# Optimization experiments

Measured on AMD Instinct MI355X. Metric: run time of the kernel, lower is better.

Reference implementation:

```python
import jax, jax.numpy as jnp
import numpy as np


def setup_inputs() -> dict:
    key = jax.random.key(0)
    ks = jax.random.split(key, 16)
    B, S, D, H = 32, 2048, 512, 512
    s = 1.0 / np.sqrt(H)
    inp = {
        "x": jax.random.normal(ks[0], (B, H), jnp.float32),
        "context": jax.random.normal(ks[1], (B, S, D), jnp.float32),
        "mask": jnp.zeros((B, S), jnp.bool_),  # False = valid position
        "Wi": jax.random.normal(ks[2], (H, H), jnp.float32) * s,
        "bi": jax.random.normal(ks[3], (H,), jnp.float32) * s,
        "Wc0": jax.random.normal(ks[4], (H, D), jnp.float32) * s,
        "bc0": jax.random.normal(ks[5], (H,), jnp.float32) * s,
        "Wc1": jax.random.normal(ks[6], (H, D), jnp.float32) * s,
        "bc1": jax.random.normal(ks[7], (H,), jnp.float32) * s,
        "Wc2": jax.random.normal(ks[8], (H, D), jnp.float32) * s,
        "bc2": jax.random.normal(ks[9], (H,), jnp.float32) * s,
        "Wc3": jax.random.normal(ks[10], (H, D), jnp.float32) * s,
        "bc3": jax.random.normal(ks[11], (H,), jnp.float32) * s,
        "V": jax.random.uniform(ks[12], (H,), jnp.float32, -s, s),
    }
    return inp


def reference(x, context, mask, Wi, bi, Wc0, bc0, Wc1, bc1, Wc2, bc2, Wc3, bc3, V):
    # mask: True = masked out in the original API; module flips it first.
    valid = ~mask  # [B, S], True = keep

    inp = (x @ Wi.T + bi)[:, :, None]  # [B, H, 1]

    def proj(W, b):
        # Conv1d(D, H, kernel=1) on context.permute(0,2,1) == token-wise GEMM
        return jnp.einsum("bsd,hd->bhs", context, W) + b[None, :, None]  # [B, H, S]

    ctx = jnp.concatenate(
        [proj(Wc0, bc0), proj(Wc1, bc1), proj(Wc2, bc2), proj(Wc3, bc3)], axis=2
    )  # [B, H, 4S]

    t = jnp.tanh(inp + ctx)                      # [B, H, 4S]
    att = jnp.einsum("h,bhs->bs", V, t)          # bmm(V[B,1,H], t).squeeze(1)
    att = 10.0 * jnp.tanh(att)                   # [B, 4S]

    valid4 = jnp.tile(valid, (1, 4))             # mask.repeat(1, 4)
    att = jnp.where(valid4, att, -jnp.inf)
    # torch.no_grad() around the masked fill detaches the rest of the graph
    att = jax.lax.stop_gradient(att)

    ans = jax.nn.softmax(att, axis=1)            # [B, 4S]
    p = jnp.max(ans, axis=1)
    indices = jnp.argmax(ans, axis=1)
    return indices[:, None], p[:, None], mask
```

## Files before the change

### kernel.cpp

```cpp
#include <hip/hip_runtime.h>
#include <math.h>

typedef __bf16 bf16x8 __attribute__((ext_vector_type(8)));
typedef float f32x4 __attribute__((ext_vector_type(4)));
typedef short short8v __attribute__((ext_vector_type(8)));

#define MARGIN 0.01f
#define NCAND 32

#define WAITL do { asm volatile("s_waitcnt lgkmcnt(0)" ::: "memory"); __builtin_amdgcn_sched_barrier(0); } while (0)
#define WAITV do { asm volatile("s_waitcnt vmcnt(0)" ::: "memory"); __builtin_amdgcn_sched_barrier(0); } while (0)
#define RBAR  do { __builtin_amdgcn_sched_barrier(0); __builtin_amdgcn_s_barrier(); } while (0)
#define BARR  __builtin_amdgcn_s_barrier()

#define MFMA_PHASE(NH, B0, B1) do { \
    WAITL; \
    __builtin_amdgcn_s_setprio(1); \
    _Pragma("unroll") \
    for (int mi = 0; mi < 8; ++mi) { \
      acc[mi][2*(NH)]   = __builtin_amdgcn_mfma_f32_16x16x32_bf16(a[mi], (B0), acc[mi][2*(NH)],   0, 0, 0); \
      acc[mi][2*(NH)+1] = __builtin_amdgcn_mfma_f32_16x16x32_bf16(a[mi], (B1), acc[mi][2*(NH)+1], 0, 0, 0); \
    } \
    __builtin_amdgcn_s_setprio(0); \
  } while (0)

__device__ __forceinline__ unsigned short f2bf(float f) {
  unsigned u = __float_as_uint(f);
  u += 0x7fffu + ((u >> 16) & 1u);
  return (unsigned short)(u >> 16);
}
__device__ __forceinline__ float tanh_fast(float x) {
  float e = __builtin_amdgcn_exp2f(x * 2.885390081777927f);
  return 1.f - 2.f * __builtin_amdgcn_rcpf(e + 1.f);
}
__device__ __forceinline__ void gl_lds16(const void* g, void* l) {
  __builtin_amdgcn_global_load_lds(
      (const __attribute__((address_space(1))) unsigned int*)g,
      (__attribute__((address_space(3))) unsigned int*)l, 16, 0, 0);
}

__global__ __launch_bounds__(256) void prep_inp_k(const float* __restrict__ x,
    const float* __restrict__ Wi, const float* __restrict__ bi, float* __restrict__ inp) {
  int gid = blockIdx.x * 256 + threadIdx.x;
  int b = gid >> 9, h = gid & 511;
  const float* xr = x + b * 512;
  const float* wr = Wi + h * 512;
  float acc = bi[h];
  #pragma unroll 4
  for (int k = 0; k < 512; k += 4) {
    float4 xv = *(const float4*)(xr + k);
    float4 wv = *(const float4*)(wr + k);
    acc += xv.x * wv.x + xv.y * wv.y + xv.z * wv.z + xv.w * wv.w;
  }
  inp[gid] = acc;
}

__global__ __launch_bounds__(256) void prep_w_pack_k(const float* __restrict__ w0,
    const float* __restrict__ w1, const float* __restrict__ w2, const float* __restrict__ w3,
    short* __restrict__ Whi) {
  int gid = blockIdx.x * 256 + threadIdx.x;
  if (gid >= 131072) return;
  int s = gid & 7, r = (gid >> 3) & 255, KT = (gid >> 11) & 7, TN = gid >> 14;
  int n = TN * 256 + r;
  int g = n >> 9, h = n & 511;
  const float* w = (g == 0) ? w0 : (g == 1) ? w1 : (g == 2) ? w2 : w3;
  int k = KT * 64 + ((s ^ (r & 7)) * 8);
  float f[8];
  *(float4*)&f[0] = *(const float4*)(w + (size_t)h * 512 + k);
  *(float4*)&f[4] = *(const float4*)(w + (size_t)h * 512 + k + 4);
  short8v hv;
  #pragma unroll
  for (int i = 0; i < 8; ++i) hv[i] = (short)f2bf(f[i]);
  *(short8v*)(Whi + (size_t)gid * 8) = hv;
}

__global__ __launch_bounds__(256) void prep_ctx_pack_k(const float* __restrict__ ctx,
    short* __restrict__ Chi) {
  int gid = blockIdx.x * 256 + threadIdx.x;
  int s = gid & 7, r = (gid >> 3) & 255, KT = (gid >> 11) & 7, TM = gid >> 14;
  size_t m = (size_t)TM * 256 + r;
  int k = KT * 64 + ((s ^ (r & 7)) * 8);
  float f[8];
  *(float4*)&f[0] = *(const float4*)(ctx + m * 512 + k);
  *(float4*)&f[4] = *(const float4*)(ctx + m * 512 + k + 4);
  short8v hv;
  #pragma unroll
  for (int i = 0; i < 8; ++i) hv[i] = (short)f2bf(f[i]);
  *(short8v*)(Chi + (size_t)gid * 8) = hv;
}

template<bool PRESPLIT>
__global__ __launch_bounds__(512, 2) void gemm_att_k(
    const float* __restrict__ ctx, const short* __restrict__ Chi,
    const short* __restrict__ Whi,
    const float* __restrict__ inp,
    const float* __restrict__ bc0, const float* __restrict__ bc1,
    const float* __restrict__ bc2, const float* __restrict__ bc3,
    const float* __restrict__ V, float* __restrict__ att) {
  __shared__ __align__(16) short smem[2][2][16384];
  __shared__ float sV[256], sPre[256];

  const int t = threadIdx.x;
  int d = blockIdx.x + (blockIdx.y << 3);
  int work = (d & 7) * 256 + (d >> 3);
  int mt = work >> 3, nt = work & 7;
  int b = mt >> 3;
  int g = nt >> 1, h0 = (nt & 1) * 256;

  if (t < 256) {
    const float* bc = (g == 0) ? bc0 : (g == 1) ? bc1 : (g == 2) ? bc2 : bc3;
    sV[t] = V[h0 + t];
    sPre[t] = inp[b * 512 + h0 + t] + bc[h0 + t];
  }

  const int toff = t * 8;
  auto stageA = [&](int tile) {
    const short* gA = Chi + ((size_t)(mt * 8 + tile)) * 16384 + toff;
    short* lA = &smem[tile & 1][0][0];
    gl_lds16(gA,         lA + toff);
    gl_lds16(gA + 4096,  lA + toff + 4096);
    gl_lds16(gA + 8192,  lA + toff + 8192);
    gl_lds16(gA + 12288, lA + toff + 12288);
  };
  auto stageB = [&](int tile) {
    const short* gB = Whi + ((size_t)(nt * 8 + tile)) * 16384 + toff;
    short* lB = &smem[tile & 1][1][0];
    gl_lds16(gB,         lB + toff);
    gl_lds16(gB + 4096,  lB + toff + 4096);
    gl_lds16(gB + 8192,  lB + toff + 8192);
    gl_lds16(gB + 12288, lB + toff + 12288);
  };
  auto stageA_reg = [&](int tile) {
    #pragma unroll
    for (int pass = 0; pass < 4; ++pass) {
      int cc = pass * 512 + t;
      int s = cc & 7, r = cc >> 3;
      int k = tile * 64 + ((s ^ (r & 7)) * 8);
      const float* src = ctx + ((size_t)mt * 256 + r) * 512 + k;
      float f[8];
      *(float4*)&f[0] = *(const float4*)src;
      *(float4*)&f[4] = *(const float4*)(src + 4);
      short8v hv;
      #pragma unroll
      for (int i = 0; i < 8; ++i) hv[i] = (short)f2bf(f[i]);
      *(short8v*)(&smem[tile & 1][0][r * 64 + s * 8]) = hv;
    }
  };

  f32x4 acc[8][4];
  #pragma unroll
  for (int i = 0; i < 8; ++i)
    #pragma unroll
    for (int j = 0; j < 4; ++j) acc[i][j] = (f32x4){0.f, 0.f, 0.f, 0.f};

  const int lane = t & 63, wid = t >> 6;
  const int wr = wid >> 2, wc = wid & 3;
  const int fr = lane & 15, fq = lane >> 4;
  const int slot = fq ^ (fr & 7);
  const int aoff = (wr * 128 + fr) * 64 + slot * 8;
  const int boff = (wc * 64 + fr) * 64 + slot * 8;

  if (PRESPLIT) stageA(0); else stageA_reg(0);
  stageB(0);
  WAITV;
  BARR;

  bf16x8 a[8];
  for (int tt = 0; tt < 8; ++tt) {
    short* sa = &smem[tt & 1][0][0];
    short* sb = &smem[tt & 1][1][0];
    const int ap1 = aoff ^ 32, bp1 = boff ^ 32;
    bf16x8 b0, b1;
    #pragma unroll
    for (int mi = 0; mi < 8; ++mi) a[mi] = *(const bf16x8*)(sa + aoff + mi * 1024);
    b0 = *(const bf16x8*)(sb + boff);
    b1 = *(const bf16x8*)(sb + boff + 1024);
    if (tt < 7) { if (PRESPLIT) stageA(tt + 1); else stageA_reg(tt + 1); }
    RBAR;
    MFMA_PHASE(0, b0, b1);
    BARR;
    b0 = *(const bf16x8*)(sb + boff + 2048);
    b1 = *(const bf16x8*)(sb + boff + 3072);
    if (tt < 7) stageB(tt + 1);
    RBAR;
    MFMA_PHASE(1, b0, b1);
    BARR;
    #pragma unroll
    for (int mi = 0; mi < 8; ++mi) a[mi] = *(const bf16x8*)(sa + ap1 + mi * 1024);
    b0 = *(const bf16x8*)(sb + bp1);
    b1 = *(const bf16x8*)(sb + bp1 + 1024);
    RBAR;
    MFMA_PHASE(0, b0, b1);
    BARR;
    b0 = *(const bf16x8*)(sb + bp1 + 2048);
    b1 = *(const bf16x8*)(sb + bp1 + 3072);
    RBAR;
    MFMA_PHASE(1, b0, b1);
    WAITV;
    BARR;
  }

  float vV[4], vP[4];
  #pragma unroll
  for (int ni = 0; ni < 4; ++ni) {
    int j = wc * 64 + ni * 16 + fr;
    vV[ni] = sV[j];
    vP[ni] = sPre[j];
  }
  size_t abase = (size_t)b * 8192 + (size_t)g * 2048;
  #pragma unroll
  for (int mi = 0; mi < 8; ++mi) {
    #pragma unroll
    for (int r = 0; r < 4; ++r) {
      float sum = 0.f;
      #pragma unroll
      for (int ni = 0; ni < 4; ++ni)
        sum += vV[ni] * tanh_fast(vP[ni] + acc[mi][ni][r]);
      sum += __shfl_xor(sum, 1, 64);
      sum += __shfl_xor(sum, 2, 64);
      sum += __shfl_xor(sum, 4, 64);
      sum += __shfl_xor(sum, 8, 64);
      if (fr == 0) {
        int s = (mt * 256 + wr * 128 + mi * 16 + fq * 4 + r) & 2047;
        atomicAdd(&att[abase + s], sum);
      }
    }
  }
}

__global__ __launch_bounds__(256) void tail_k(const float* __restrict__ att,
    const unsigned char* __restrict__ mask, const float* __restrict__ ctx,
    const float* __restrict__ Wc0, const float* __restrict__ Wc1,
    const float* __restrict__ Wc2, const float* __restrict__ Wc3,
    const float* __restrict__ bc0, const float* __restrict__ bc1,
    const float* __restrict__ bc2, const float* __restrict__ bc3,
    const float* __restrict__ inp, const float* __restrict__ V,
    float* __restrict__ out) {
  int b = blockIdx.x, t = threadIdx.x;
  __shared__ float sred[256];
  __shared__ float sctx[512];
  __shared__ int scnt;
  __shared__ int scand_j[NCAND];
  __shared__ float scand_a[NCAND];
  __shared__ float sexact[NCAND];

  if (t == 0) scnt = 0;
  float bm = -1e30f;
  for (int j = t; j < 8192; j += 256) {
    if (mask[b * 2048 + (j & 2047)]) continue;
    bm = fmaxf(bm, att[(size_t)b * 8192 + j]);
  }
  sred[t] = bm;
  __syncthreads();
  for (int s2 = 128; s2 > 0; s2 >>= 1) {
    if (t < s2) sred[t] = fmaxf(sred[t], sred[t + s2]);
    __syncthreads();
  }
  float mx = sred[0];
  float Lref = 10.f * tanhf(mx);
  __syncthreads();
  float se = 0.f;
  for (int j = t; j < 8192; j += 256) {
    if (mask[b * 2048 + (j & 2047)]) continue;
    float a = att[(size_t)b * 8192 + j];
    se += expf(10.f * tanhf(a) - Lref);
    if (a >= mx - MARGIN) {
      int slot = atomicAdd(&scnt, 1);
      if (slot < NCAND) { scand_j[slot] = j; scand_a[slot] = a; }
    }
  }
  sred[t] = se;
  __syncthreads();
  for (int s2 = 128; s2 > 0; s2 >>= 1) {
    if (t < s2) sred[t] += sred[t + s2];
    __syncthreads();
  }
  float den = sred[0];
  int n = min(scnt, NCAND);
  for (int j = t; j < 2048; j += 256)
    out[64 + b * 2048 + j] = mask[b * 2048 + j] ? 1.0f : 0.0f;
  for (int i = 0; i < n; ++i) {
    int jj = scand_j[i];
    int g = jj >> 11, s = jj & 2047;
    const float* W  = (g == 0) ? Wc0 : (g == 1) ? Wc1 : (g == 2) ? Wc2 : Wc3;
    const float* bc = (g == 0) ? bc0 : (g == 1) ? bc1 : (g == 2) ? bc2 : bc3;
    const float* cr = ctx + ((size_t)b * 2048 + s) * 512;
    __syncthreads();
    sctx[t] = cr[t];
    sctx[t + 256] = cr[t + 256];
    __syncthreads();
    float total = 0.f;
    #pragma unroll
    for (int hh = 0; hh < 2; ++hh) {
      int h = t + hh * 256;
      const float* wrp = W + (size_t)h * 512;
      float acc = 0.f;
      #pragma unroll 4
      for (int k = 0; k < 512; k += 4) {
        float4 wv = *(const float4*)(wrp + k);
        acc += wv.x * sctx[k] + wv.y * sctx[k + 1] + wv.z * sctx[k + 2] + wv.w * sctx[k + 3];
      }
      total += V[h] * tanhf(inp[b * 512 + h] + bc[h] + acc);
    }
    sred[t] = total;
    __syncthreads();
    for (int s2 = 128; s2 > 0; s2 >>= 1) {
      if (t < s2) sred[t] += sred[t + s2];
      __syncthreads();
    }
    if (t == 0) sexact[i] = sred[0];
  }
  __syncthreads();
  if (t == 0) {
    float dd = den, best = -1e30f;
    int bj = 0x7fffffff;
    for (int i = 0; i < n; ++i) {
      float e = sexact[i];
      int j = scand_j[i];
      dd += expf(10.f * tanhf(e) - Lref) - expf(10.f * tanhf(scand_a[i]) - Lref);
      if (e > best || (e == best && j < bj)) { best = e; bj = j; }
    }
    out[b] = (float)bj;
    out[32 + b] = expf(10.f * tanhf(best) - Lref) / dd;
  }
}

extern "C" void kernel_launch(void* const* d_in, const int* in_sizes, int n_in,
                              void* d_out, int out_size, void* d_ws, size_t ws_size,
                              hipStream_t stream) {
  const float* x    = (const float*)d_in[0];
  const float* ctx  = (const float*)d_in[1];
  const unsigned char* mask = (const unsigned char*)d_in[2];
  const float* Wi   = (const float*)d_in[3];
  const float* bi   = (const float*)d_in[4];
  const float* Wc0  = (const float*)d_in[5];
  const float* bc0  = (const float*)d_in[6];
  const float* Wc1  = (const float*)d_in[7];
  const float* bc1  = (const float*)d_in[8];
  const float* Wc2  = (const float*)d_in[9];
  const float* bc2  = (const float*)d_in[10];
  const float* Wc3  = (const float*)d_in[11];
  const float* bc3  = (const float*)d_in[12];
  const float* V    = (const float*)d_in[13];
  float* out = (float*)d_out;

  float* inp    = (float*)d_ws;
  float* att    = inp + 16384;
  short* Whi    = (short*)(att + 262144);
  short* Chi    = Whi + 1048576;
  size_t need = (size_t)((char*)(Chi + 33554432) - (char*)d_ws);
  bool presplit = ws_size >= need;

  hipMemsetAsync(att, 0, 262144 * sizeof(float), stream);
  prep_inp_k<<<64, 256, 0, stream>>>(x, Wi, bi, inp);
  prep_w_pack_k<<<512, 256, 0, stream>>>(Wc0, Wc1, Wc2, Wc3, Whi);
  if (presplit) {
    prep_ctx_pack_k<<<16384, 256, 0, stream>>>(ctx, Chi);
    gemm_att_k<true><<<dim3(8, 256), 512, 0, stream>>>(ctx, Chi, Whi,
        inp, bc0, bc1, bc2, bc3, V, att);
  } else {
    gemm_att_k<false><<<dim3(8, 256), 512, 0, stream>>>(ctx, nullptr, Whi,
        inp, bc0, bc1, bc2, bc3, V, att);
  }
  tail_k<<<32, 256, 0, stream>>>(att, mask, ctx, Wc0, Wc1, Wc2, Wc3,
      bc0, bc1, bc2, bc3, inp, V, out);
}
```

Baseline: 325.2 us.

## Deepen GEMM pipeline to 4-stage ring with K=32 tiles and prefetch distance 3

The bf16 GEMM now uses K-tiles of 32 instead of 64, stored in a 4-deep LDS ring buffer, and issues global-to-LDS loads three tiles ahead. Partial vmcnt waits let several tiles of loads stay in flight at once. The prepacked layouts and the XOR swizzle are reworked to match the 32-wide rows. The aim is to hide global memory latency better. The cost is twice as many barriers per unit of K and smaller MFMA bursts between syncs.

```diff
diff --git a/kernel.cpp b/kernel.cpp
--- a/kernel.cpp
+++ b/kernel.cpp
@@ -8,10 +8,12 @@
 #define MARGIN 0.01f
 #define NCAND 32
 
-#define WAITL do { asm volatile("s_waitcnt lgkmcnt(0)" ::: "memory"); __builtin_amdgcn_sched_barrier(0); } while (0)
-#define WAITV do { asm volatile("s_waitcnt vmcnt(0)" ::: "memory"); __builtin_amdgcn_sched_barrier(0); } while (0)
-#define RBAR  do { __builtin_amdgcn_sched_barrier(0); __builtin_amdgcn_s_barrier(); } while (0)
-#define BARR  __builtin_amdgcn_s_barrier()
+#define WAITL  do { asm volatile("s_waitcnt lgkmcnt(0)" ::: "memory"); __builtin_amdgcn_sched_barrier(0); } while (0)
+#define WAITV0 do { asm volatile("s_waitcnt vmcnt(0)" ::: "memory"); __builtin_amdgcn_sched_barrier(0); } while (0)
+#define WAITV4 do { asm volatile("s_waitcnt vmcnt(4)" ::: "memory"); __builtin_amdgcn_sched_barrier(0); } while (0)
+#define WAITV8 do { asm volatile("s_waitcnt vmcnt(8)" ::: "memory"); __builtin_amdgcn_sched_barrier(0); } while (0)
+#define RBAR   do { __builtin_amdgcn_sched_barrier(0); __builtin_amdgcn_s_barrier(); } while (0)
+#define BARR   __builtin_amdgcn_s_barrier()
 
 #define MFMA_PHASE(NH, B0, B1) do { \
     WAITL; \
@@ -60,14 +62,16 @@
     short* __restrict__ Whi) {
   int gid = blockIdx.x * 256 + threadIdx.x;
   if (gid >= 131072) return;
-  int s = gid & 7, r = (gid >> 3) & 255, KT = (gid >> 11) & 7, TN = gid >> 14;
-  int n = TN * 256 + r;
+  int c = gid & 3, row = (gid >> 2) & 255, TK = gid >> 10;
+  int TN = TK >> 4, KS = TK & 15;
+  int n = TN * 256 + row;
   int g = n >> 9, h = n & 511;
   const float* w = (g == 0) ? w0 : (g == 1) ? w1 : (g == 2) ? w2 : w3;
-  int k = KT * 64 + ((s ^ (r & 7)) * 8);
+  int csrc = c ^ ((row >> 1) & 3);
+  const float* src = w + (size_t)h * 512 + KS * 32 + csrc * 8;
   float f[8];
-  *(float4*)&f[0] = *(const float4*)(w + (size_t)h * 512 + k);
-  *(float4*)&f[4] = *(const float4*)(w + (size_t)h * 512 + k + 4);
+  *(float4*)&f[0] = *(const float4*)(src);
+  *(float4*)&f[4] = *(const float4*)(src + 4);
   short8v hv;
   #pragma unroll
   for (int i = 0; i < 8; ++i) hv[i] = (short)f2bf(f[i]);
@@ -77,9 +81,11 @@
 __global__ __launch_bounds__(256) void prep_ctx_pack_k(const float* __restrict__ ctx,
     short* __restrict__ Chi) {
   int gid = blockIdx.x * 256 + threadIdx.x;
-  int s = gid & 7, r = (gid >> 3) & 255, KT = (gid >> 11) & 7, TM = gid >> 14;
-  size_t m = (size_t)TM * 256 + r;
-  int k = KT * 64 + ((s ^ (r & 7)) * 8);
+  int c = gid & 3, row = (gid >> 2) & 255, TK = gid >> 10;
+  int TM = TK >> 4, KS = TK & 15;
+  size_t m = (size_t)TM * 256 + row;
+  int csrc = c ^ ((row >> 1) & 3);
+  int k = KS * 32 + csrc * 8;
   float f[8];
   *(float4*)&f[0] = *(const float4*)(ctx + m * 512 + k);
   *(float4*)&f[4] = *(const float4*)(ctx + m * 512 + k + 4);
@@ -97,7 +103,7 @@
     const float* __restrict__ bc0, const float* __restrict__ bc1,
     const float* __restrict__ bc2, const float* __restrict__ bc3,
     const float* __restrict__ V, float* __restrict__ att) {
-  __shared__ __align__(16) short smem[2][2][16384];
+  __shared__ __align__(16) short smem[4][2][8192];
   __shared__ float sV[256], sPre[256];
 
   const int t = threadIdx.x;
@@ -115,27 +121,24 @@
 
   const int toff = t * 8;
   auto stageA = [&](int tile) {
-    const short* gA = Chi + ((size_t)(mt * 8 + tile)) * 16384 + toff;
-    short* lA = &smem[tile & 1][0][0];
-    gl_lds16(gA,         lA + toff);
-    gl_lds16(gA + 4096,  lA + toff + 4096);
-    gl_lds16(gA + 8192,  lA + toff + 8192);
-    gl_lds16(gA + 12288, lA + toff + 12288);
+    const short* gA = Chi + (((size_t)mt * 16 + tile) << 13) + toff;
+    short* lA = &smem[tile & 3][0][0];
+    gl_lds16(gA,        lA + toff);
+    gl_lds16(gA + 4096, lA + toff + 4096);
   };
   auto stageB = [&](int tile) {
-    const short* gB = Whi + ((size_t)(nt * 8 + tile)) * 16384 + toff;
-    short* lB = &smem[tile & 1][1][0];
-    gl_lds16(gB,         lB + toff);
-    gl_lds16(gB + 4096,  lB + toff + 4096);
-    gl_lds16(gB + 8192,  lB + toff + 8192);
-    gl_lds16(gB + 12288, lB + toff + 12288);
+    const short* gB = Whi + (((size_t)nt * 16 + tile) << 13) + toff;
+    short* lB = &smem[tile & 3][1][0];
+    gl_lds16(gB,        lB + toff);
+    gl_lds16(gB + 4096, lB + toff + 4096);
   };
   auto stageA_reg = [&](int tile) {
     #pragma unroll
-    for (int pass = 0; pass < 4; ++pass) {
+    for (int pass = 0; pass < 2; ++pass) {
       int cc = pass * 512 + t;
-      int s = cc & 7, r = cc >> 3;
-      int k = tile * 64 + ((s ^ (r & 7)) * 8);
+      int c = cc & 3, r = cc >> 2;
+      int csrc = c ^ ((r >> 1) & 3);
+      int k = tile * 32 + csrc * 8;
       const float* src = ctx + ((size_t)mt * 256 + r) * 512 + k;
       float f[8];
       *(float4*)&f[0] = *(const float4*)src;
@@ -143,7 +146,7 @@
       short8v hv;
       #pragma unroll
       for (int i = 0; i < 8; ++i) hv[i] = (short)f2bf(f[i]);
-      *(short8v*)(&smem[tile & 1][0][r * 64 + s * 8]) = hv;
+      *(short8v*)(&smem[tile & 3][0][r * 32 + c * 8]) = hv;
     }
   };
 
@@ -156,47 +159,47 @@
   const int lane = t & 63, wid = t >> 6;
   const int wr = wid >> 2, wc = wid & 3;
   const int fr = lane & 15, fq = lane >> 4;
-  const int slot = fq ^ (fr & 7);
-  const int aoff = (wr * 128 + fr) * 64 + slot * 8;
-  const int boff = (wc * 64 + fr) * 64 + slot * 8;
-
-  if (PRESPLIT) stageA(0); else stageA_reg(0);
-  stageB(0);
-  WAITV;
+  const int csw = fq ^ ((fr >> 1) & 3);
+  const int abase = (wr * 128 + fr) * 32 + csw * 8;
+  const int bbase = (wc * 64 + fr) * 32 + csw * 8;
+
+  if constexpr (PRESPLIT) {
+    stageA(0); stageB(0); stageA(1); stageB(1); stageA(2); stageB(2);
+    WAITV8;
+  } else {
+    stageA_reg(0); stageB(0);
+    WAITV0;
+  }
   BARR;
 
-  bf16x8 a[8];
-  for (int tt = 0; tt < 8; ++tt) {
-    short* sa = &smem[tt & 1][0][0];
-    short* sb = &smem[tt & 1][1][0];
-    const int ap1 = aoff ^ 32, bp1 = boff ^ 32;
-    bf16x8 b0, b1;
-    #pragma unroll
-    for (int mi = 0; mi < 8; ++mi) a[mi] = *(const bf16x8*)(sa + aoff + mi * 1024);
-    b0 = *(const bf16x8*)(sb + boff);
-    b1 = *(const bf16x8*)(sb + boff + 1024);
-    if (tt < 7) { if (PRESPLIT) stageA(tt + 1); else stageA_reg(tt + 1); }
+  #pragma unroll
+  for (int tt = 0; tt < 16; ++tt) {
+    const short* sa = &smem[tt & 3][0][0];
+    const short* sb = &smem[tt & 3][1][0];
+    bf16x8 a[8], b0, b1;
+    #pragma unroll
+    for (int mi = 0; mi < 8; ++mi)
+      a[mi] = *(const bf16x8*)(sa + abase + mi * 512);
+    b0 = *(const bf16x8*)(sb + bbase);
+    b1 = *(const bf16x8*)(sb + bbase + 512);
+    if constexpr (PRESPLIT) { if (tt < 13) stageA(tt + 3); }
+    else                    { if (tt < 15) stageA_reg(tt + 1); }
     RBAR;
     MFMA_PHASE(0, b0, b1);
     BARR;
-    b0 = *(const bf16x8*)(sb + boff + 2048);
-    b1 = *(const bf16x8*)(sb + boff + 3072);
-    if (tt < 7) stageB(tt + 1);
+    b0 = *(const bf16x8*)(sb + bbase + 1024);
+    b1 = *(const bf16x8*)(sb + bbase + 1536);
+    if constexpr (PRESPLIT) { if (tt < 13) stageB(tt + 3); }
+    else                    { if (tt < 15) stageB(tt + 1); }
     RBAR;
     MFMA_PHASE(1, b0, b1);
-    BARR;
-    #pragma unroll
-    for (int mi = 0; mi < 8; ++mi) a[mi] = *(const bf16x8*)(sa + ap1 + mi * 1024);
-    b0 = *(const bf16x8*)(sb + bp1);
-    b1 = *(const bf16x8*)(sb + bp1 + 1024);
-    RBAR;
-    MFMA_PHASE(0, b0, b1);
-    BARR;
-    b0 = *(const bf16x8*)(sb + bp1 + 2048);
-    b1 = *(const bf16x8*)(sb + bp1 + 3072);
-    RBAR;
-    MFMA_PHASE(1, b0, b1);
-    WAITV;
+    if constexpr (PRESPLIT) {
+      if (tt <= 12) { WAITV8; }
+      else if (tt == 13) { WAITV4; }
+      else if (tt == 14) { WAITV0; }
+    } else {
+      if (tt < 15) { WAITV0; }
+    }
     BARR;
   }
 
@@ -207,7 +210,7 @@
     vV[ni] = sV[j];
     vP[ni] = sPre[j];
   }
-  size_t abase = (size_t)b * 8192 + (size_t)g * 2048;
+  size_t abatt = (size_t)b * 8192 + (size_t)g * 2048;
   #pragma unroll
   for (int mi = 0; mi < 8; ++mi) {
     #pragma unroll
@@ -222,7 +225,7 @@
       sum += __shfl_xor(sum, 8, 64);
       if (fr == 0) {
         int s = (mt * 256 + wr * 128 + mi * 16 + fq * 4 + r) & 2047;
-        atomicAdd(&att[abase + s], sum);
+        atomicAdd(&att[abatt + s], sum);
       }
     }
   }
```

Measured after the change: 322.3 us. Within noise of the previous version (-0.9%).
